# Kernel optimization log

Hardware: AMD Instinct MI355X
Metric: run time of the kernel (lower is better)

## Reference

```python
import jax, jax.numpy as jnp
import numpy as np

H, W = 512, 512
N_POINTS = 4194304


def setup_inputs() -> dict:
    key = jax.random.key(0)
    k1, k2 = jax.random.split(key)
    # point coordinates in [0, 510) so trunc()+1 <= 511 stays in-bounds
    point = jax.random.uniform(k1, (1, N_POINTS, 2), dtype=jnp.float32) * 510.0
    flow = jax.random.normal(k2, (1, 2, H, W), dtype=jnp.float32)
    return {"point": point, "flow": flow, "intep": 1}


def _normalized_locs(flow):
    # grid buffer: torch.meshgrid defaults to 'ij' indexing -> [2, H, W]
    gy, gx = jnp.meshgrid(jnp.arange(H, dtype=jnp.float32),
                          jnp.arange(W, dtype=jnp.float32), indexing="ij")
    grid = jnp.stack([gy, gx])[None]            # [1, 2, H, W]
    nl = grid + flow                            # [1, 2, H, W]
    nl0 = 2.0 * (nl[:, 0] / (H - 1) - 0.5)      # normalized row coord
    nl1 = 2.0 * (nl[:, 1] / (W - 1) - 0.5)      # normalized col coord
    # permute(0,2,3,1) then channel swap [...,[1,0]] -> last dim = (nl1, nl0)
    return jnp.stack([nl1, nl0], axis=-1)[0]    # [H, W, 2]


def reference(point, flow, intep):
    L = _normalized_locs(flow)                  # [H, W, 2]
    x = point[0, :, 0]                          # [N]
    y = point[0, :, 1]
    if intep:
        xt = jnp.trunc(x); xf = x - xt          # frac() = x - trunc(x)
        yt = jnp.trunc(y); yf = y - yt
        x0 = xt.astype(jnp.int32); y0 = yt.astype(jnp.int32)
        x1 = x0 + 1;                y1 = y0 + 1
        v00 = L[x0, y0]  # weight xf*yf        (dic['0'])
        v10 = L[x1, y0]  # weight xf*(1-yf)    (dic['1'])
        v01 = L[x0, y1]  # weight (1-xf)*yf    (dic['2'])
        v11 = L[x1, y1]  # weight (1-xf)*(1-yf)(dic['3'])
        w00 = (xf * yf)[:, None]
        w10 = (xf * (1.0 - yf))[:, None]
        w01 = ((1.0 - xf) * yf)[:, None]
        w11 = ((1.0 - xf) * (1.0 - yf))[:, None]
        tmp = w00 * v00 + w10 * v10 + w01 * v01 + w11 * v11  # [N, 2]
    else:
        xi = jnp.minimum(jnp.round(x), 511.0).astype(jnp.int32)
        yi = jnp.minimum(jnp.round(y), 511.0).astype(jnp.int32)
        tmp = L[xi, yi]                          # [N, 2]
    # new_point[...,1] <- from channel 0 (tmp_x); new_point[...,0] <- channel 1
    out0 = (tmp[:, 1] + 1.0) / 2.0 * 512.0
    out1 = (tmp[:, 0] + 1.0) / 2.0 * 512.0
    return jnp.stack([out0, out1], axis=-1)[None]  # [1, N, 2]
```

## Files before the change

### kernel.cpp

```cpp
#include <hip/hip_runtime.h>
#include <hip/hip_fp16.h>


constexpr int HH = 512;
constexpr int WW = 512;

typedef float f32x4 __attribute__((ext_vector_type(4)));

__device__ __forceinline__ float Lx_val(const float* __restrict__ flow, int i, int j) {
    const float s = 2.0f / 511.0f;
    return fmaf((float)j + flow[(i << 9) + j + HH * WW], s, -1.0f);
}
__device__ __forceinline__ float Ly_val(const float* __restrict__ flow, int i, int j) {
    const float s = 2.0f / 511.0f;
    return fmaf((float)i + flow[(i << 9) + j], s, -1.0f);
}

__device__ __forceinline__ unsigned int pack_corner(const float* __restrict__ flow,
                                                    int i, int j) {
    __half2 h = __float22half2_rn(make_float2(Lx_val(flow, i, j), Ly_val(flow, i, j)));
    return *reinterpret_cast<unsigned int*>(&h);
}

__global__ __launch_bounds__(256) void build_T_kernel(const float* __restrict__ flow,
                                                      uint4* __restrict__ T) {
    int idx = blockIdx.x * 256 + threadIdx.x;
    int i = idx >> 9;
    int j = idx & 511;
    int ip = min(i + 1, 511);
    int jp = min(j + 1, 511);
    uint4 e;
    e.x = pack_corner(flow, i,  j);
    e.y = pack_corner(flow, i,  jp);
    e.z = pack_corner(flow, ip, j);
    e.w = pack_corner(flow, ip, jp);
    T[idx] = e;
}

__device__ __forceinline__ float2 h2f(unsigned int u) {
    __half2 h = *reinterpret_cast<__half2*>(&u);
    float2 f = __half22float2(h);
    return f;
}

__device__ __forceinline__ float2 process_point_tbl(float x, float y, bool bil,
                                                    const uint4* __restrict__ T) {
    float2 tmp;
    if (bil) {
        float xt = truncf(x), yt = truncf(y);
        float xf = x - xt, yf = y - yt;
        int x0 = (int)xt, y0 = (int)yt;
        uint4 e = T[(x0 << 9) + y0];
        float2 v00 = h2f(e.x);
        float2 v01 = h2f(e.y);
        float2 v10 = h2f(e.z);
        float2 v11 = h2f(e.w);
        float w00 = xf * yf;
        float w10 = xf * (1.0f - yf);
        float w01 = (1.0f - xf) * yf;
        float w11 = (1.0f - xf) * (1.0f - yf);
        tmp.x = w00 * v00.x + w10 * v10.x + w01 * v01.x + w11 * v11.x;
        tmp.y = w00 * v00.y + w10 * v10.y + w01 * v01.y + w11 * v11.y;
    } else {
        int xi = min((int)rintf(x), 511);
        int yi = min((int)rintf(y), 511);
        uint4 e = T[(xi << 9) + yi];
        tmp = h2f(e.x);
    }
    return make_float2((tmp.y + 1.0f) * 256.0f,
                       (tmp.x + 1.0f) * 256.0f);
}

__device__ __forceinline__ float2 load_L_direct(const float* __restrict__ flow,
                                                int x, int y) {
    return make_float2(Lx_val(flow, x, y), Ly_val(flow, x, y));
}

__device__ __forceinline__ float2 process_point_direct(float x, float y, bool bil,
                                                       const float* __restrict__ flow) {
    float2 tmp;
    if (bil) {
        float xt = truncf(x), yt = truncf(y);
        float xf = x - xt, yf = y - yt;
        int x0 = (int)xt, y0 = (int)yt;
        float2 v00 = load_L_direct(flow, x0,     y0);
        float2 v01 = load_L_direct(flow, x0,     y0 + 1);
        float2 v10 = load_L_direct(flow, x0 + 1, y0);
        float2 v11 = load_L_direct(flow, x0 + 1, y0 + 1);
        float w00 = xf * yf;
        float w10 = xf * (1.0f - yf);
        float w01 = (1.0f - xf) * yf;
        float w11 = (1.0f - xf) * (1.0f - yf);
        tmp.x = w00 * v00.x + w10 * v10.x + w01 * v01.x + w11 * v11.x;
        tmp.y = w00 * v00.y + w10 * v10.y + w01 * v01.y + w11 * v11.y;
    } else {
        int xi = min((int)rintf(x), 511);
        int yi = min((int)rintf(y), 511);
        tmp = load_L_direct(flow, xi, yi);
    }
    return make_float2((tmp.y + 1.0f) * 256.0f,
                       (tmp.x + 1.0f) * 256.0f);
}

template <bool USE_TABLE>
__global__ __launch_bounds__(256) void pst_kernel(const float* __restrict__ point,
                                                  const uint4* __restrict__ T,
                                                  const float* __restrict__ flow,
                                                  const int* __restrict__ intep,
                                                  float* __restrict__ out,
                                                  int n ) {
    const bool bil = (*intep != 0);
    const int npairs = n >> 1;
    int tid = blockIdx.x * blockDim.x + threadIdx.x;
    int stride = gridDim.x * blockDim.x;

    const f32x4* pts4 = reinterpret_cast<const f32x4*>(point);
    f32x4* out4 = reinterpret_cast<f32x4*>(out);

    for (int i = tid; i < npairs; i += stride) {
        f32x4 p = __builtin_nontemporal_load(&pts4[i]);
        float2 r0, r1;
        if constexpr (USE_TABLE) {
            r0 = process_point_tbl(p.x, p.y, bil, T);
            r1 = process_point_tbl(p.z, p.w, bil, T);
        } else {
            r0 = process_point_direct(p.x, p.y, bil, flow);
            r1 = process_point_direct(p.z, p.w, bil, flow);
        }
        f32x4 r = {r0.x, r0.y, r1.x, r1.y};
        __builtin_nontemporal_store(r, &out4[i]);
    }
    if ((n & 1) && tid == 0) {
        const float2* pt2 = reinterpret_cast<const float2*>(point);
        float2 p = pt2[n - 1];
        float2 r;
        if constexpr (USE_TABLE) r = process_point_tbl(p.x, p.y, bil, T);
        else                     r = process_point_direct(p.x, p.y, bil, flow);
        reinterpret_cast<float2*>(out)[n - 1] = r;
    }
}

extern "C" void kernel_launch(void* const* d_in, const int* in_sizes, int n_in,
                              void* d_out, int out_size, void* d_ws, size_t ws_size,
                              hipStream_t stream) {
    const float* point = (const float*)d_in[0];
    const float* flow  = (const float*)d_in[1];
    const int*   intep = (const int*)d_in[2];
    float* out = (float*)d_out;

    const int n = in_sizes[0] / 2;
    const int npairs = n >> 1;

    const size_t table_bytes = (size_t)HH * WW * sizeof(uint4);
    const bool use_table = (ws_size >= table_bytes);

    int blocks = (npairs + 255) / 256;
    if (blocks > 2048) blocks = 2048;
    if (blocks < 1) blocks = 1;

    if (use_table) {
        uint4* T = (uint4*)d_ws;
        build_T_kernel<<<HH * WW / 256, 256, 0, stream>>>(flow, T);
        pst_kernel<true><<<blocks, 256, 0, stream>>>(point, T, flow, intep, out, n);
    } else {
        pst_kernel<false><<<blocks, 256, 0, stream>>>(point, nullptr, flow, intep, out, n);
    }
}
```

Before: 114.9 us.

## Process eight points per thread with batched table gathers and no grid-stride loop

The point kernel now gives each thread eight points. It loads them as four vector loads, issues all eight table gathers together behind a scheduling barrier, then computes and stores. The aim is to raise memory-level parallelism and hide gather latency. The grid-stride loop with capped blocks is replaced by one thread per eight points, and the direct-flow fallback is removed, so the table workspace is now assumed to exist. The point loads are no longer nontemporal, and more registers are needed per thread.

```diff
diff --git a/kernel.cpp b/kernel.cpp
--- a/kernel.cpp
+++ b/kernel.cpp
@@ -39,104 +39,106 @@
 
 __device__ __forceinline__ float2 h2f(unsigned int u) {
     __half2 h = *reinterpret_cast<__half2*>(&u);
-    float2 f = __half22float2(h);
-    return f;
+    return __half22float2(h);
 }
 
-__device__ __forceinline__ float2 process_point_tbl(float x, float y, bool bil,
-                                                    const uint4* __restrict__ T) {
-    float2 tmp;
+__device__ __forceinline__ float2 combine4(uint4 e, float xf, float yf) {
+    float2 v00 = h2f(e.x);
+    float2 v01 = h2f(e.y);
+    float2 v10 = h2f(e.z);
+    float2 v11 = h2f(e.w);
+    float w00 = xf * yf;
+    float w10 = xf * (1.0f - yf);
+    float w01 = (1.0f - xf) * yf;
+    float w11 = (1.0f - xf) * (1.0f - yf);
+    float tx = w00 * v00.x + w10 * v10.x + w01 * v01.x + w11 * v11.x;
+    float ty = w00 * v00.y + w10 * v10.y + w01 * v01.y + w11 * v11.y;
+    return make_float2((ty + 1.0f) * 256.0f, (tx + 1.0f) * 256.0f);
+}
+
+__device__ __forceinline__ float2 point_scalar(const uint4* __restrict__ T,
+                                               float x, float y, bool bil) {
     if (bil) {
         float xt = truncf(x), yt = truncf(y);
-        float xf = x - xt, yf = y - yt;
         int x0 = (int)xt, y0 = (int)yt;
-        uint4 e = T[(x0 << 9) + y0];
-        float2 v00 = h2f(e.x);
-        float2 v01 = h2f(e.y);
-        float2 v10 = h2f(e.z);
-        float2 v11 = h2f(e.w);
-        float w00 = xf * yf;
-        float w10 = xf * (1.0f - yf);
-        float w01 = (1.0f - xf) * yf;
-        float w11 = (1.0f - xf) * (1.0f - yf);
-        tmp.x = w00 * v00.x + w10 * v10.x + w01 * v01.x + w11 * v11.x;
-        tmp.y = w00 * v00.y + w10 * v10.y + w01 * v01.y + w11 * v11.y;
+        return combine4(T[(x0 << 9) + y0], x - xt, y - yt);
     } else {
         int xi = min((int)rintf(x), 511);
         int yi = min((int)rintf(y), 511);
-        uint4 e = T[(xi << 9) + yi];
-        tmp = h2f(e.x);
+        float2 t = h2f(T[(xi << 9) + yi].x);
+        return make_float2((t.y + 1.0f) * 256.0f, (t.x + 1.0f) * 256.0f);
     }
-    return make_float2((tmp.y + 1.0f) * 256.0f,
-                       (tmp.x + 1.0f) * 256.0f);
 }
 
-__device__ __forceinline__ float2 load_L_direct(const float* __restrict__ flow,
-                                                int x, int y) {
-    return make_float2(Lx_val(flow, x, y), Ly_val(flow, x, y));
-}
+__global__ __launch_bounds__(256, 2) void pst_kernel(const float* __restrict__ point,
+                                                     const uint4* __restrict__ T,
+                                                     const int* __restrict__ intep,
+                                                     float* __restrict__ out,
+                                                     int n ) {
+    const bool bil = (*intep != 0);
+    int tid = blockIdx.x * 256 + threadIdx.x;
+    int base = tid * 8;
 
-__device__ __forceinline__ float2 process_point_direct(float x, float y, bool bil,
-                                                       const float* __restrict__ flow) {
-    float2 tmp;
-    if (bil) {
-        float xt = truncf(x), yt = truncf(y);
-        float xf = x - xt, yf = y - yt;
-        int x0 = (int)xt, y0 = (int)yt;
-        float2 v00 = load_L_direct(flow, x0,     y0);
-        float2 v01 = load_L_direct(flow, x0,     y0 + 1);
-        float2 v10 = load_L_direct(flow, x0 + 1, y0);
-        float2 v11 = load_L_direct(flow, x0 + 1, y0 + 1);
-        float w00 = xf * yf;
-        float w10 = xf * (1.0f - yf);
-        float w01 = (1.0f - xf) * yf;
-        float w11 = (1.0f - xf) * (1.0f - yf);
-        tmp.x = w00 * v00.x + w10 * v10.x + w01 * v01.x + w11 * v11.x;
-        tmp.y = w00 * v00.y + w10 * v10.y + w01 * v01.y + w11 * v11.y;
-    } else {
-        int xi = min((int)rintf(x), 511);
-        int yi = min((int)rintf(y), 511);
-        tmp = load_L_direct(flow, xi, yi);
-    }
-    return make_float2((tmp.y + 1.0f) * 256.0f,
-                       (tmp.x + 1.0f) * 256.0f);
-}
+    if (base + 7 < n) {
+        const f32x4* pts  = reinterpret_cast<const f32x4*>(point);
+        f32x4*       out4 = reinterpret_cast<f32x4*>(out);
+        f32x4 p0 = pts[tid * 4 + 0];
+        f32x4 p1 = pts[tid * 4 + 1];
+        f32x4 p2 = pts[tid * 4 + 2];
+        f32x4 p3 = pts[tid * 4 + 3];
+        float x[8] = {p0.x, p0.z, p1.x, p1.z, p2.x, p2.z, p3.x, p3.z};
+        float y[8] = {p0.y, p0.w, p1.y, p1.w, p2.y, p2.w, p3.y, p3.w};
 
-template <bool USE_TABLE>
-__global__ __launch_bounds__(256) void pst_kernel(const float* __restrict__ point,
-                                                  const uint4* __restrict__ T,
-                                                  const float* __restrict__ flow,
-                                                  const int* __restrict__ intep,
-                                                  float* __restrict__ out,
-                                                  int n ) {
-    const bool bil = (*intep != 0);
-    const int npairs = n >> 1;
-    int tid = blockIdx.x * blockDim.x + threadIdx.x;
-    int stride = gridDim.x * blockDim.x;
+        if (bil) {
+            float xf[8], yf[8];
+            int idx[8];
+#pragma unroll
+            for (int k = 0; k < 8; ++k) {
+                float xt = truncf(x[k]), yt = truncf(y[k]);
+                xf[k] = x[k] - xt;
+                yf[k] = y[k] - yt;
+                idx[k] = ((int)xt << 9) + (int)yt;
+            }
+            uint4 e[8];
+#pragma unroll
+            for (int k = 0; k < 8; ++k) e[k] = T[idx[k]];
+            __builtin_amdgcn_sched_barrier(0);
 
-    const f32x4* pts4 = reinterpret_cast<const f32x4*>(point);
-    f32x4* out4 = reinterpret_cast<f32x4*>(out);
+            float2 r[8];
+#pragma unroll
+            for (int k = 0; k < 8; ++k) r[k] = combine4(e[k], xf[k], yf[k]);
 
-    for (int i = tid; i < npairs; i += stride) {
-        f32x4 p = __builtin_nontemporal_load(&pts4[i]);
-        float2 r0, r1;
-        if constexpr (USE_TABLE) {
-            r0 = process_point_tbl(p.x, p.y, bil, T);
-            r1 = process_point_tbl(p.z, p.w, bil, T);
+#pragma unroll
+            for (int q = 0; q < 4; ++q) {
+                f32x4 o = {r[2 * q].x, r[2 * q].y, r[2 * q + 1].x, r[2 * q + 1].y};
+                __builtin_nontemporal_store(o, &out4[tid * 4 + q]);
+            }
         } else {
-            r0 = process_point_direct(p.x, p.y, bil, flow);
-            r1 = process_point_direct(p.z, p.w, bil, flow);
+            const unsigned int* Tw = reinterpret_cast<const unsigned int*>(T);
+            unsigned int v[8];
+#pragma unroll
+            for (int k = 0; k < 8; ++k) {
+                int xi = min((int)rintf(x[k]), 511);
+                int yi = min((int)rintf(y[k]), 511);
+                v[k] = Tw[(((xi << 9) + yi) << 2)];
+            }
+            __builtin_amdgcn_sched_barrier(0);
+#pragma unroll
+            for (int q = 0; q < 4; ++q) {
+                float2 ta = h2f(v[2 * q]);
+                float2 tb = h2f(v[2 * q + 1]);
+                f32x4 o = {(ta.y + 1.0f) * 256.0f, (ta.x + 1.0f) * 256.0f,
+                           (tb.y + 1.0f) * 256.0f, (tb.x + 1.0f) * 256.0f};
+                __builtin_nontemporal_store(o, &out4[tid * 4 + q]);
+            }
         }
-        f32x4 r = {r0.x, r0.y, r1.x, r1.y};
-        __builtin_nontemporal_store(r, &out4[i]);
-    }
-    if ((n & 1) && tid == 0) {
-        const float2* pt2 = reinterpret_cast<const float2*>(point);
-        float2 p = pt2[n - 1];
-        float2 r;
-        if constexpr (USE_TABLE) r = process_point_tbl(p.x, p.y, bil, T);
-        else                     r = process_point_direct(p.x, p.y, bil, flow);
-        reinterpret_cast<float2*>(out)[n - 1] = r;
+    } else if (base < n) {
+        const float2* pt2  = reinterpret_cast<const float2*>(point);
+        float2*       out2 = reinterpret_cast<float2*>(out);
+        for (int k = base; k < n; ++k) {
+            float2 p = pt2[k];
+            out2[k] = point_scalar(T, p.x, p.y, bil);
+        }
     }
 }
 
@@ -149,20 +151,13 @@
     float* out = (float*)d_out;
 
     const int n = in_sizes[0] / 2;
-    const int npairs = n >> 1;
 
-    const size_t table_bytes = (size_t)HH * WW * sizeof(uint4);
-    const bool use_table = (ws_size >= table_bytes);
+    uint4* T = (uint4*)d_ws;
 
-    int blocks = (npairs + 255) / 256;
-    if (blocks > 2048) blocks = 2048;
+    build_T_kernel<<<HH * WW / 256, 256, 0, stream>>>(flow, T);
+
+    int nthreads = (n + 7) / 8;
+    int blocks = (nthreads + 255) / 256;
     if (blocks < 1) blocks = 1;
-
-    if (use_table) {
-        uint4* T = (uint4*)d_ws;
-        build_T_kernel<<<HH * WW / 256, 256, 0, stream>>>(flow, T);
-        pst_kernel<true><<<blocks, 256, 0, stream>>>(point, T, flow, intep, out, n);
-    } else {
-        pst_kernel<false><<<blocks, 256, 0, stream>>>(point, nullptr, flow, intep, out, n);
-    }
+    pst_kernel<<<blocks, 256, 0, stream>>>(point, T, intep, out, n);
 }
```

After: 128.4 us. 11.7% more time.
